# Performance work log

Measured on AMD Instinct MI355X. Metric: run time of the kernel, lower is better.

Reference implementation:

```python
import jax, jax.numpy as jnp
import numpy as np

CUTOFF = 5.0
RBF_DIM = 32
M0, M1, M2 = 128, 64, 32          # node multiplicities for l=0,1,2
DIM_NODE = M0 + 3 * M1 + 5 * M2   # 480
MSG = 64                          # message multiplicity per l
NBLK = 3
MAX_Z = 100


def _sph_harm(d):
    # component-normalized real spherical harmonics up to lmax=2; d: [E,3] unit vectors
    x, y, z = d[:, 0], d[:, 1], d[:, 2]
    s3, s5, s15 = jnp.sqrt(3.0), jnp.sqrt(5.0), jnp.sqrt(15.0)
    return jnp.stack([
        jnp.ones_like(x),
        s3 * x, s3 * y, s3 * z,
        s15 * x * y, s15 * y * z, 0.5 * s5 * (3.0 * z * z - 1.0),
        s15 * x * z, 0.5 * s15 * (x * x - y * y),
    ], axis=-1)  # [E, 9]


def _rbf(d):
    centers = jnp.linspace(0.0, CUTOFF, RBF_DIM)
    width = CUTOFF / (RBF_DIM - 1)
    return jnp.exp(-0.5 * ((d[:, None] - centers) / width) ** 2)  # [E, RBF_DIM]


def _irrep_norm(x):
    # per-node RMS norm of each irrep block (l=0,1,2)
    eps = 1e-6
    parts = []
    for off, mul, dim in ((0, M0, 1), (M0, M1, 3), (M0 + 3 * M1, M2, 5)):
        blk = x[:, off:off + mul * dim].reshape(-1, mul, dim)
        rms = jnp.sqrt(jnp.mean(jnp.sum(blk * blk, axis=-1), axis=-1, keepdims=True) + eps)
        parts.append((blk / rms[..., None]).reshape(-1, mul * dim))
    return jnp.concatenate(parts, axis=-1)


def setup_inputs() -> dict:
    key = jax.random.key(0)
    ks = jax.random.split(key, 20)
    B, N, E = 32, 128, 131072
    BN = B * N

    z = jax.random.randint(ks[0], (B, N), 1, MAX_Z + 1)
    mask = jnp.ones((B, N), jnp.float32)
    edge_src = jax.random.randint(ks[1], (E,), 0, BN)
    edge_dst = jax.random.randint(ks[2], (E,), 0, BN)
    edge_weight = jax.random.uniform(ks[3], (E,), minval=0.1, maxval=CUTOFF)
    ed = jax.random.normal(ks[4], (E, 3), jnp.float32)
    ed = ed / jnp.linalg.norm(ed, axis=-1, keepdims=True)
    edge_vec = ed * edge_weight[:, None]

    def nrm(k, shape, fan_in):
        return jax.random.normal(k, shape, jnp.float32) / np.sqrt(fan_in)

    params = {
        "z_emb": jax.random.normal(ks[5], (MAX_Z + 1, M0), jnp.float32),
        "W_in": nrm(ks[6], (M0, M0), M0),
        "Wp": nrm(ks[7], (NBLK, M0, 3 * MSG), M0),
        "rW1": nrm(ks[8], (NBLK, RBF_DIM, 64), RBF_DIM),
        "rb1": jnp.zeros((NBLK, 64), jnp.float32),
        "rW2": nrm(ks[9], (NBLK, 64, 3 * MSG), 64),
        "rb2": jnp.zeros((NBLK, 3 * MSG), jnp.float32),
        "Wo0": nrm(ks[10], (NBLK, MSG, M0), MSG),
        "Wo1": nrm(ks[11], (NBLK, MSG, M1), MSG),
        "Wo2": nrm(ks[12], (NBLK, MSG, M2), MSG),
        "res_scale": jnp.full((NBLK,), 1.0, jnp.float32),
    }
    return {"z": z, "mask": mask, "edge_src": edge_src, "edge_dst": edge_dst,
            "edge_weight": edge_weight, "edge_vec": edge_vec, **params}


def reference(z, mask, edge_src, edge_dst, edge_weight, edge_vec,
              z_emb, W_in, Wp, rW1, rb1, rW2, rb2, Wo0, Wo1, Wo2, res_scale):
    B, N = z.shape
    BN = B * N
    fmask = mask.reshape(BN)

    # element embedding -> o3.Linear(0e -> irreps_node): only scalar channels are produced
    zf = z_emb[z.reshape(BN)]                                    # [BN, node_attr]
    x0 = zf @ W_in                                               # [BN, M0]
    x = jnp.concatenate([x0, jnp.zeros((BN, DIM_NODE - M0), x0.dtype)], axis=-1)
    x = x * fmask[:, None]

    elen = edge_weight
    edir = edge_vec / jnp.clip(elen, 1e-8)[:, None]
    rbf = _rbf(jnp.minimum(elen, CUTOFF))                        # [E, RBF_DIM]
    sh = _sph_harm(edir)                                         # [E, 9]
    fcut = 0.5 * (jnp.cos(jnp.pi * jnp.minimum(elen / CUTOFF, 1.0)) + 1.0)

    for b in range(NBLK):
        s = x[:, :M0]
        proj = s[edge_src] @ Wp[b]                               # [E, 3*MSG] gather + GEMM
        h = jax.nn.silu(rbf @ rW1[b] + rb1[b])
        r = h @ rW2[b] + rb2[b]                                  # [E, 3*MSG] radial weights
        w = proj * r * fcut[:, None]
        w0, w1, w2 = w[:, :MSG], w[:, MSG:2 * MSG], w[:, 2 * MSG:]
        msg0 = w0 * sh[:, 0:1]                                   # [E, MSG]
        msg1 = w1[:, :, None] * sh[:, None, 1:4]                 # [E, MSG, 3]
        msg2 = w2[:, :, None] * sh[:, None, 4:9]                 # [E, MSG, 5]
        m0 = jax.ops.segment_sum(msg0, edge_dst, num_segments=BN)
        m1 = jax.ops.segment_sum(msg1, edge_dst, num_segments=BN)
        m2 = jax.ops.segment_sum(msg2, edge_dst, num_segments=BN)
        u0 = m0 @ Wo0[b]                                         # [BN, M0]
        u1 = jnp.einsum('ncd,ck->nkd', m1, Wo1[b]).reshape(BN, 3 * M1)
        u2 = jnp.einsum('ncd,ck->nkd', m2, Wo2[b]).reshape(BN, 5 * M2)
        x = x + res_scale[b] * jnp.concatenate([u0, u1, u2], axis=-1)

    x = _irrep_norm(x) * fmask[:, None]
    return x.reshape(B, N, DIM_NODE)
```

## Files before the change

### kernel.cpp

```cpp
#include <hip/hip_runtime.h>
#include <math.h>

#define M0 128
#define M1 64
#define M2 32
#define DIMN 480
#define MSGC 64
#define NBLK 3
#define RBFD 32
#define NT 512
#define TCHUNK 32
#define NNP0 4
#define GNPB 4
#define PSTR 68
#define WROWS 224
#define FCUT 5.0f

typedef unsigned int   u32;
typedef unsigned short u16;

__device__ __forceinline__ u16 f2bf(float f) {
    u32 u = __float_as_uint(f);
    u32 r = (u + 0x7fffu + ((u >> 16) & 1u)) >> 16;
    return (u16)r;
}
__device__ __forceinline__ float bf_lo(u32 v) { return __uint_as_float(v << 16); }
__device__ __forceinline__ float bf_hi(u32 v) { return __uint_as_float(v & 0xffff0000u); }

struct __align__(16) ERec {
    int   src;
    int   ti;
    float fr;
    float fc;
    float sh[8];
};

__global__ void k_zero(int* __restrict__ p, int n) {
    int i = blockIdx.x * blockDim.x + threadIdx.x;
    if (i < n) p[i] = 0;
}

__global__ void k_count(const int* __restrict__ dst, int* __restrict__ counts, int E) {
    int e = blockIdx.x * blockDim.x + threadIdx.x;
    if (e >= E) return;
    atomicAdd(&counts[dst[e]], 1);
}

__global__ __launch_bounds__(1024) void k_scan(const int* __restrict__ counts,
                                               int* __restrict__ offs,
                                               int* __restrict__ cursor, int n) {
    __shared__ int ws[1024];
    int t = threadIdx.x;
    int4 v = ((const int4*)counts)[t];
    int s0 = v.x, s1 = s0 + v.y, s2 = s1 + v.z, s3 = s2 + v.w;
    ws[t] = s3;
    __syncthreads();
    for (int d = 1; d < 1024; d <<= 1) {
        int val = (t >= d) ? ws[t - d] : 0;
        __syncthreads();
        ws[t] += val;
        __syncthreads();
    }
    int excl = (t == 0) ? 0 : ws[t - 1];
    int4 o;
    o.x = excl; o.y = excl + s0; o.z = excl + s1; o.w = excl + s2;
    ((int4*)offs)[t] = o;
    ((int4*)cursor)[t] = o;
    if (t == 1023) offs[n] = excl + s3;
}

__global__ void k_build(const float* __restrict__ ew, const float* __restrict__ ev,
                        const int* __restrict__ src, const int* __restrict__ dst,
                        int* __restrict__ cursor, ERec* __restrict__ rec, int E) {
    int e = blockIdx.x * blockDim.x + threadIdx.x;
    if (e >= E) return;
    float len = ew[e];
    float inv = 1.0f / fmaxf(len, 1e-8f);
    float x = ev[e * 3 + 0] * inv;
    float y = ev[e * 3 + 1] * inv;
    float z = ev[e * 3 + 2] * inv;
    const float s3 = 1.7320508075688772f, s5 = 2.23606797749979f, s15 = 3.872983346207417f;
    ERec r;
    r.src = src[e];
    float u = fminf(len, FCUT) * ((float)(NT - 1) / FCUT);
    int ti = (int)u;
    ti = min(ti, NT - 2);
    r.ti = ti;
    r.fr = u - (float)ti;
    float t = fminf(len / FCUT, 1.0f);
    float fc = 0.5f * (cosf(3.14159265358979323846f * t) + 1.0f);
    r.fc = fc;
    r.sh[0] = s3 * x * fc;
    r.sh[1] = s3 * y * fc;
    r.sh[2] = s3 * z * fc;
    r.sh[3] = s15 * x * y * fc;
    r.sh[4] = s15 * y * z * fc;
    r.sh[5] = 0.5f * s5 * (3.0f * z * z - 1.0f) * fc;
    r.sh[6] = s15 * x * z * fc;
    r.sh[7] = 0.5f * s15 * (x * x - y * y) * fc;
    int p = atomicAdd(&cursor[dst[e]], 1);
    rec[p] = r;
}

#define RTB (NBLK * (NT / TCHUNK))
__global__ __launch_bounds__(256) void k_rtab(const float* __restrict__ rW1,
                                              const float* __restrict__ rb1,
                                              const float* __restrict__ rW2,
                                              const float* __restrict__ rb2,
                                              u32* __restrict__ rPI,
                                              const float* __restrict__ Wo0,
                                              const float* __restrict__ Wo1,
                                              const float* __restrict__ Wo2,
                                              float* __restrict__ WoT) {
    int blk = blockIdx.x;
    int tid = threadIdx.x;
    if (blk >= RTB) {
        int idx = (blk - RTB) * 256 + tid;
        const int wtot = NBLK * WROWS * 64;
        if (idx >= wtot) return;
        int b = idx / (WROWS * 64);
        int rem = idx - b * (WROWS * 64);
        int row = rem >> 6, c = rem & 63;
        float v;
        if (row < 128)      v = Wo0[(size_t)b * MSGC * M0 + c * M0 + row];
        else if (row < 192) v = Wo1[(size_t)b * MSGC * M1 + c * M1 + (row - 128)];
        else                v = Wo2[(size_t)b * MSGC * M2 + c * M2 + (row - 192)];
        WoT[idx] = v;
        return;
    }
    int b = blk / (NT / TCHUNK);
    int t0 = (blk % (NT / TCHUNK)) * TCHUNK;
    __shared__ float rbf_s[TCHUNK + 1][RBFD];
    __shared__ float hh_s[64][TCHUNK + 1];

    const float wdt = FCUT / (float)(RBFD - 1);
    for (int idx = tid; idx < (TCHUNK + 1) * RBFD; idx += 256) {
        int tt = idx >> 5, k = idx & 31;
        int te = min(t0 + tt, NT - 1);
        float len = (float)te * (FCUT / (float)(NT - 1));
        float d0 = (len - (float)k * wdt) / wdt;
        rbf_s[tt][k] = expf(-0.5f * d0 * d0);
    }
    __syncthreads();
    const float* W1 = rW1 + b * RBFD * 64;
    for (int idx = tid; idx < (TCHUNK + 1) * 64; idx += 256) {
        int tt = idx / 64, jj = idx & 63;
        float a = rb1[b * 64 + jj];
        #pragma unroll 8
        for (int k = 0; k < RBFD; ++k) a += rbf_s[tt][k] * W1[k * 64 + jj];
        hh_s[jj][tt] = a / (1.0f + expf(-a));
    }
    __syncthreads();
    if (tid < 192) {
        int c = tid;
        const float* W2 = rW2 + b * 64 * 192;
        float w2r[64];
        #pragma unroll
        for (int k = 0; k < 64; ++k) w2r[k] = W2[k * 192 + c];
        float b2 = rb2[b * 192 + c];
        int lane = c & 63, q = c >> 6;
        u32* out = rPI + ((size_t)b * NT * 64) * 4;
        float prev = 0.0f;
        for (int tt = 0; tt <= TCHUNK; ++tt) {
            float acc = b2;
            #pragma unroll
            for (int k = 0; k < 64; ++k) acc += hh_s[k][tt] * w2r[k];
            if (tt > 0) {
                int t = t0 + tt - 1;
                out[((size_t)t * 64 + lane) * 4 + q] =
                    (u32)f2bf(prev) | ((u32)f2bf(acc) << 16);
            }
            prev = acc;
        }
    }
}

__global__ __launch_bounds__(192) void k_proj0(const int* __restrict__ z,
                                               const float* __restrict__ mask,
                                               const float* __restrict__ zemb,
                                               const float* __restrict__ Win,
                                               const float* __restrict__ Wp,
                                               float* __restrict__ x,
                                               u16* __restrict__ PI) {
    int n0 = blockIdx.x * NNP0;
    int j = threadIdx.x;
    __shared__ float zf[NNP0][M0];
    __shared__ float xs[NNP0][M0];
    for (int idx = j; idx < NNP0 * M0; idx += 192) {
        int n = idx >> 7, c = idx & 127;
        zf[n][c] = zemb[z[n0 + n] * M0 + c];
    }
    __syncthreads();
    for (int idx = j; idx < NNP0 * M0; idx += 192) {
        int n = idx >> 7, c = idx & 127;
        float acc = 0.0f;
        for (int k = 0; k < M0; ++k) acc += zf[n][k] * Win[k * M0 + c];
        acc *= mask[n0 + n];
        xs[n][c] = acc;
        x[(size_t)(n0 + n) * DIMN + c] = acc;
    }
    for (int idx = j; idx < NNP0 * (DIMN - M0); idx += 192) {
        int n = idx / (DIMN - M0), c = idx - n * (DIMN - M0);
        x[(size_t)(n0 + n) * DIMN + M0 + c] = 0.0f;
    }
    __syncthreads();
    float acc[NNP0];
    #pragma unroll
    for (int u = 0; u < NNP0; ++u) acc[u] = 0.0f;
    for (int k = 0; k < M0; ++k) {
        float wv = Wp[k * 192 + j];
        #pragma unroll
        for (int u = 0; u < NNP0; ++u) acc[u] += xs[u][k] * wv;
    }
    int lane = j & 63, q = j >> 6;
    #pragma unroll
    for (int u = 0; u < NNP0; ++u)
        PI[((size_t)(n0 + u) * 64 + lane) * 4 + q] = f2bf(acc[u]);
}

__global__ __launch_bounds__(512) void k_gather(const u16* __restrict__ PIin,
                                                u16* __restrict__ PIout,
                                                const u32* __restrict__ rPI,
                                                const ERec* __restrict__ rec,
                                                const int* __restrict__ offs,
                                                const float* __restrict__ WoT,
                                                const float* __restrict__ WpNext,
                                                const float* __restrict__ res_scale, int b,
                                                float* __restrict__ x,
                                                const float* __restrict__ mask,
                                                float* __restrict__ out) {
    int t = threadIdx.x;
    int w = t >> 6;
    int j = t & 63;
    int local = w >> 1;
    int par = w & 1;
    int n0 = blockIdx.x * GNPB;
    int n = n0 + local;
    int e0 = offs[n], e1 = offs[n + 1];

    float m0 = 0.0f;
    float m1a[3] = {0, 0, 0};
    float m2a[5] = {0, 0, 0, 0, 0};

    __shared__ float mbuf[8][9 * PSTR];
    __shared__ float invs[GNPB][3];

    {
        int i0 = e0 + par;
        if (i0 < e1) {
            const int last = e1 - 1;
            int nIter = (e1 - i0 + 1) >> 1;
            float4 A0, A1, A2, B0, B1, B2, C0, C1, C2;
            {
                int ia = __builtin_amdgcn_readfirstlane(i0);
                const float4* p = (const float4*)(rec + ia);
                A0 = p[0]; A1 = p[1]; A2 = p[2];
            }
            {
                int v = i0 + 2; v = v < e1 ? v : last;
                int ib = __builtin_amdgcn_readfirstlane(v);
                const float4* p = (const float4*)(rec + ib);
                B0 = p[0]; B1 = p[1]; B2 = p[2];
            }
            {
                int v = i0 + 4; v = v < e1 ? v : last;
                int ic = __builtin_amdgcn_readfirstlane(v);
                const float4* p = (const float4*)(rec + ic);
                C0 = p[0]; C1 = p[1]; C2 = p[2];
            }
            uint4 rA, rB, rC; uint2 pA, pB, pC;
            {
                int s = __float_as_int(A0.x), ti = __float_as_int(A0.y);
                rA = ((const uint4*)(rPI + ((size_t)ti << 8)))[j];
                pA = ((const uint2*)(PIin + ((size_t)s << 8)))[j];
            }
            {
                int s = __float_as_int(B0.x), ti = __float_as_int(B0.y);
                rB = ((const uint4*)(rPI + ((size_t)ti << 8)))[j];
                pB = ((const uint2*)(PIin + ((size_t)s << 8)))[j];
            }
            #pragma unroll 4
            for (int k = 0; k < nIter; ++k) {
                int i = i0 + (k << 1);
                float4 D0, D1, D2;
                {
                    int v = i + 6; v = v < e1 ? v : last;
                    int id = __builtin_amdgcn_readfirstlane(v);
                    const float4* p = (const float4*)(rec + id);
                    D0 = p[0]; D1 = p[1]; D2 = p[2];
                }
                {
                    int s = __float_as_int(C0.x), ti = __float_as_int(C0.y);
                    rC = ((const uint4*)(rPI + ((size_t)ti << 8)))[j];
                    pC = ((const uint2*)(PIin + ((size_t)s << 8)))[j];
                }
                float fr = A0.z, fc = A0.w;
                float la = bf_lo(rA.x);
                float va = la + fr * (bf_hi(rA.x) - la);
                float p0 = __uint_as_float(pA.x << 16);
                float p1 = __uint_as_float(pA.x & 0xffff0000u);
                float p2 = __uint_as_float(pA.y << 16);
                m0 = fmaf(p0 * va, fc, m0);
                float lb = bf_lo(rA.y);
                float vb = lb + fr * (bf_hi(rA.y) - lb);
                float w1 = p1 * vb;
                m1a[0] += w1 * A1.x;
                m1a[1] += w1 * A1.y;
                m1a[2] += w1 * A1.z;
                float lc = bf_lo(rA.z);
                float vc = lc + fr * (bf_hi(rA.z) - lc);
                float w2 = p2 * vc;
                m2a[0] += w2 * A1.w;
                m2a[1] += w2 * A2.x;
                m2a[2] += w2 * A2.y;
                m2a[3] += w2 * A2.z;
                m2a[4] += w2 * A2.w;
                A0 = B0; A1 = B1; A2 = B2;
                B0 = C0; B1 = C1; B2 = C2;
                C0 = D0; C1 = D1; C2 = D2;
                rA = rB; pA = pB; rB = rC; pB = pC;
            }
        }
    }

    mbuf[w][0 * PSTR + j] = m0;
    #pragma unroll
    for (int d = 0; d < 3; ++d) mbuf[w][(1 + d) * PSTR + j] = m1a[d];
    #pragma unroll
    for (int d = 0; d < 5; ++d) mbuf[w][(4 + d) * PSTR + j] = m2a[d];
    __syncthreads();
    #pragma unroll
    for (int u = 0; u < GNPB; ++u)
        for (int c = t; c < 9 * PSTR; c += 512)
            mbuf[2 * u][c] += mbuf[2 * u + 1][c];
    __syncthreads();

    float rs = res_scale[b];
    int o = t;
    if (o < DIMN) {
        int row, mbase;
        if (o < M0) {
            row = o; mbase = 0;
        } else if (o < M0 + 3 * M1) {
            int q = o - M0, k = q / 3, d = q - 3 * k;
            row = 128 + k; mbase = (1 + d) * PSTR;
        } else {
            int q = o - (M0 + 3 * M1), k = q / 5, d = q - 5 * k;
            row = 192 + k; mbase = (4 + d) * PSTR;
        }
        const float4* Wv = (const float4*)(WoT + (size_t)row * 64);
        float a0 = 0, a1 = 0, a2 = 0, a3 = 0;
        #pragma unroll
        for (int c4 = 0; c4 < 16; ++c4) {
            float4 wv = Wv[c4];
            float4 v0 = *(const float4*)&mbuf[0][mbase + 4 * c4];
            float4 v1 = *(const float4*)&mbuf[2][mbase + 4 * c4];
            float4 v2 = *(const float4*)&mbuf[4][mbase + 4 * c4];
            float4 v3 = *(const float4*)&mbuf[6][mbase + 4 * c4];
            a0 += wv.x * v0.x + wv.y * v0.y + wv.z * v0.z + wv.w * v0.w;
            a1 += wv.x * v1.x + wv.y * v1.y + wv.z * v1.z + wv.w * v1.w;
            a2 += wv.x * v2.x + wv.y * v2.y + wv.z * v2.z + wv.w * v2.w;
            a3 += wv.x * v3.x + wv.y * v3.y + wv.z * v3.z + wv.w * v3.w;
        }
        a0 = x[(size_t)(n0 + 0) * DIMN + o] + rs * a0;
        a1 = x[(size_t)(n0 + 1) * DIMN + o] + rs * a1;
        a2 = x[(size_t)(n0 + 2) * DIMN + o] + rs * a2;
        a3 = x[(size_t)(n0 + 3) * DIMN + o] + rs * a3;
        if (b < NBLK - 1) {
            x[(size_t)(n0 + 0) * DIMN + o] = a0;
            x[(size_t)(n0 + 1) * DIMN + o] = a1;
            x[(size_t)(n0 + 2) * DIMN + o] = a2;
            x[(size_t)(n0 + 3) * DIMN + o] = a3;
            if (o < M0) {
                mbuf[1][o] = a0; mbuf[3][o] = a1; mbuf[5][o] = a2; mbuf[7][o] = a3;
            }
        } else {
            mbuf[1][o] = a0; mbuf[3][o] = a1; mbuf[5][o] = a2; mbuf[7][o] = a3;
        }
    }

    if (b < NBLK - 1) {
        __syncthreads();
        for (int oo = t; oo < GNPB * 192; oo += 512) {
            int u = oo / 192, c = oo - u * 192;
            const float* xf = mbuf[2 * u + 1];
            float acc = 0.0f;
            #pragma unroll 8
            for (int k = 0; k < M0; ++k) acc += xf[k] * WpNext[k * 192 + c];
            PIout[((size_t)(n0 + u) * 64 + (c & 63)) * 4 + (c >> 6)] = f2bf(acc);
        }
        return;
    }

    __syncthreads();
    if (w < GNPB) {
        const float* xf = mbuf[2 * w + 1];
        float s0 = 0, s1 = 0, s2 = 0;
        for (int c = j; c < DIMN; c += 64) {
            float v = xf[c];
            if (c < 128) s0 += v * v;
            else if (c < 320) s1 += v * v;
            else s2 += v * v;
        }
        #pragma unroll
        for (int d = 32; d > 0; d >>= 1) {
            s0 += __shfl_down(s0, d);
            s1 += __shfl_down(s1, d);
            s2 += __shfl_down(s2, d);
        }
        if (j == 0) {
            invs[w][0] = rsqrtf(s0 / (float)M0 + 1e-6f);
            invs[w][1] = rsqrtf(s1 / (float)M1 + 1e-6f);
            invs[w][2] = rsqrtf(s2 / (float)M2 + 1e-6f);
        }
    }
    __syncthreads();
    if (o < DIMN) {
        int cls = (o < 128) ? 0 : (o < 320) ? 1 : 2;
        #pragma unroll
        for (int u = 0; u < GNPB; ++u) {
            float fm = mask[n0 + u];
            out[(size_t)(n0 + u) * DIMN + o] = mbuf[2 * u + 1][o] * invs[u][cls] * fm;
        }
    }
}

extern "C" void kernel_launch(void* const* d_in, const int* in_sizes, int n_in,
                              void* d_out, int out_size, void* d_ws, size_t ws_size,
                              hipStream_t stream) {
    const int*   z    = (const int*)d_in[0];
    const float* mask = (const float*)d_in[1];
    const int*   esrc = (const int*)d_in[2];
    const int*   edst = (const int*)d_in[3];
    const float* ew   = (const float*)d_in[4];
    const float* ev   = (const float*)d_in[5];
    const float* zemb = (const float*)d_in[6];
    const float* Win  = (const float*)d_in[7];
    const float* Wp   = (const float*)d_in[8];
    const float* rW1  = (const float*)d_in[9];
    const float* rb1  = (const float*)d_in[10];
    const float* rW2  = (const float*)d_in[11];
    const float* rb2  = (const float*)d_in[12];
    const float* Wo0  = (const float*)d_in[13];
    const float* Wo1  = (const float*)d_in[14];
    const float* Wo2  = (const float*)d_in[15];
    const float* res  = (const float*)d_in[16];

    const int BN = in_sizes[0];
    const int E  = in_sizes[2];

    char* w = (char*)d_ws;
    float* x    = (float*)w;  w += (size_t)BN * DIMN * 4;
    u16*   PIa  = (u16*)w;    w += (size_t)BN * 256 * 2;
    u16*   PIb  = (u16*)w;    w += (size_t)BN * 256 * 2;
    u32*   rPI  = (u32*)w;    w += (size_t)NBLK * NT * 256 * 4;
    ERec*  rec  = (ERec*)w;   w += (size_t)E * sizeof(ERec);
    float* WoT  = (float*)w;  w += (size_t)NBLK * WROWS * 64 * 4;
    int* counts = (int*)w;   w += (size_t)BN * 4;
    int* offs   = (int*)w;   w += (size_t)(BN + 4) * 4;
    int* cursor = (int*)w;   w += (size_t)BN * 4;

    k_zero<<<(BN + 255) / 256, 256, 0, stream>>>(counts, BN);
    k_count<<<(E + 255) / 256, 256, 0, stream>>>(edst, counts, E);
    k_scan<<<1, 1024, 0, stream>>>(counts, offs, cursor, BN);
    k_build<<<(E + 255) / 256, 256, 0, stream>>>(ew, ev, esrc, edst, cursor, rec, E);
    {
        int wotb = (NBLK * WROWS * 64 + 255) / 256;
        k_rtab<<<RTB + wotb, 256, 0, stream>>>(rW1, rb1, rW2, rb2, rPI,
                                               Wo0, Wo1, Wo2, WoT);
    }
    k_proj0<<<BN / NNP0, 192, 0, stream>>>(z, mask, zemb, Win, Wp, x, PIa);

    u16* pibuf[2] = {PIa, PIb};
    for (int b = 0; b < NBLK; ++b) {
        const float* WpNext = Wp + (size_t)(b + 1 < NBLK ? b + 1 : 0) * M0 * 192;
        k_gather<<<BN / GNPB, 512, 0, stream>>>(pibuf[b & 1], pibuf[(b + 1) & 1],
                                                rPI + (size_t)b * NT * 256,
                                                rec, offs,
                                                WoT + (size_t)b * WROWS * 64,
                                                WpNext, res, b, x, mask, (float*)d_out);
    }
}
```

Measured before the change: 201.7 us.

## Stage edge records in double-buffered LDS chunks and split edges contiguously per wave

Each wave now loads its edge records cooperatively in chunks of 21 into a double-buffered LDS array, instead of making per-edge scalar global loads with a deep register rotation. Edges are split into two contiguous halves per wave pair rather than interleaved by parity. The change also adds a launch-bounds occupancy hint of 6 and halves TCHUNK. It aims to cut scalar load latency and register pressure, at the cost of extra LDS traffic and chunk-boundary pipeline restarts that reissue the first two gathers of each chunk.

```diff
diff --git a/kernel.cpp b/kernel.cpp
--- a/kernel.cpp
+++ b/kernel.cpp
@@ -9,11 +9,12 @@
 #define NBLK 3
 #define RBFD 32
 #define NT 512
-#define TCHUNK 32
+#define TCHUNK 16
 #define NNP0 4
 #define GNPB 4
 #define PSTR 68
 #define WROWS 224
+#define CH 21
 #define FCUT 5.0f
 
 typedef unsigned int   u32;
@@ -218,17 +219,17 @@
         PI[((size_t)(n0 + u) * 64 + lane) * 4 + q] = f2bf(acc[u]);
 }
 
-__global__ __launch_bounds__(512) void k_gather(const u16* __restrict__ PIin,
-                                                u16* __restrict__ PIout,
-                                                const u32* __restrict__ rPI,
-                                                const ERec* __restrict__ rec,
-                                                const int* __restrict__ offs,
-                                                const float* __restrict__ WoT,
-                                                const float* __restrict__ WpNext,
-                                                const float* __restrict__ res_scale, int b,
-                                                float* __restrict__ x,
-                                                const float* __restrict__ mask,
-                                                float* __restrict__ out) {
+__global__ __launch_bounds__(512, 6) void k_gather(const u16* __restrict__ PIin,
+                                                   u16* __restrict__ PIout,
+                                                   const u32* __restrict__ rPI,
+                                                   const ERec* __restrict__ rec,
+                                                   const int* __restrict__ offs,
+                                                   const float* __restrict__ WoT,
+                                                   const float* __restrict__ WpNext,
+                                                   const float* __restrict__ res_scale, int b,
+                                                   float* __restrict__ x,
+                                                   const float* __restrict__ mask,
+                                                   float* __restrict__ out) {
     int t = threadIdx.x;
     int w = t >> 6;
     int j = t & 63;
@@ -242,83 +243,80 @@
     float m1a[3] = {0, 0, 0};
     float m2a[5] = {0, 0, 0, 0, 0};
 
+    __shared__ float4 smeta[8][2][CH * 3];
     __shared__ float mbuf[8][9 * PSTR];
     __shared__ float invs[GNPB][3];
 
     {
-        int i0 = e0 + par;
-        if (i0 < e1) {
-            const int last = e1 - 1;
-            int nIter = (e1 - i0 + 1) >> 1;
-            float4 A0, A1, A2, B0, B1, B2, C0, C1, C2;
+        int half = (e1 - e0 + 1) >> 1;
+        int a    = e0 + par * half;
+        int bnd  = par ? e1 : (e0 + half);
+        int len  = bnd - a;
+        if (len > 0) {
+            const float4* RP = (const float4*)rec;
             {
-                int ia = __builtin_amdgcn_readfirstlane(i0);
-                const float4* p = (const float4*)(rec + ia);
-                A0 = p[0]; A1 = p[1]; A2 = p[2];
+                int c0 = min(CH, len);
+                if (j < c0 * 3) smeta[w][0][j] = RP[(size_t)3 * a + j];
             }
-            {
-                int v = i0 + 2; v = v < e1 ? v : last;
-                int ib = __builtin_amdgcn_readfirstlane(v);
-                const float4* p = (const float4*)(rec + ib);
-                B0 = p[0]; B1 = p[1]; B2 = p[2];
-            }
-            {
-                int v = i0 + 4; v = v < e1 ? v : last;
-                int ic = __builtin_amdgcn_readfirstlane(v);
-                const float4* p = (const float4*)(rec + ic);
-                C0 = p[0]; C1 = p[1]; C2 = p[2];
-            }
-            uint4 rA, rB, rC; uint2 pA, pB, pC;
-            {
-                int s = __float_as_int(A0.x), ti = __float_as_int(A0.y);
-                rA = ((const uint4*)(rPI + ((size_t)ti << 8)))[j];
-                pA = ((const uint2*)(PIin + ((size_t)s << 8)))[j];
-            }
-            {
-                int s = __float_as_int(B0.x), ti = __float_as_int(B0.y);
-                rB = ((const uint4*)(rPI + ((size_t)ti << 8)))[j];
-                pB = ((const uint2*)(PIin + ((size_t)s << 8)))[j];
-            }
-            #pragma unroll 4
-            for (int k = 0; k < nIter; ++k) {
-                int i = i0 + (k << 1);
-                float4 D0, D1, D2;
+            int buf = 0;
+            for (int done = 0; done < len; done += CH, buf ^= 1) {
+                int cnt = min(CH, len - done);
                 {
-                    int v = i + 6; v = v < e1 ? v : last;
-                    int id = __builtin_amdgcn_readfirstlane(v);
-                    const float4* p = (const float4*)(rec + id);
-                    D0 = p[0]; D1 = p[1]; D2 = p[2];
+                    int nd = done + CH;
+                    int ncnt = min(CH, len - nd);
+                    if (j < ncnt * 3) smeta[w][buf ^ 1][j] = RP[(size_t)3 * (a + nd) + j];
+                }
+                const float4* M = smeta[w][buf];
+                int lastE = cnt - 1;
+                float4 Am = M[0];
+                float4 Bm = M[3 * min(1, lastE)];
+                float4 Cm = M[3 * min(2, lastE)];
+                float4 Dm = M[3 * min(3, lastE)];
+                uint4 rA, rB, rC; uint2 pA, pB, pC;
+                {
+                    int s = __float_as_int(Am.x), ti = __float_as_int(Am.y);
+                    rA = ((const uint4*)(rPI + ((size_t)ti << 8)))[j];
+                    pA = ((const uint2*)(PIin + ((size_t)s << 8)))[j];
                 }
                 {
-                    int s = __float_as_int(C0.x), ti = __float_as_int(C0.y);
-                    rC = ((const uint4*)(rPI + ((size_t)ti << 8)))[j];
-                    pC = ((const uint2*)(PIin + ((size_t)s << 8)))[j];
+                    int s = __float_as_int(Bm.x), ti = __float_as_int(Bm.y);
+                    rB = ((const uint4*)(rPI + ((size_t)ti << 8)))[j];
+                    pB = ((const uint2*)(PIin + ((size_t)s << 8)))[j];
                 }
-                float fr = A0.z, fc = A0.w;
-                float la = bf_lo(rA.x);
-                float va = la + fr * (bf_hi(rA.x) - la);
-                float p0 = __uint_as_float(pA.x << 16);
-                float p1 = __uint_as_float(pA.x & 0xffff0000u);
-                float p2 = __uint_as_float(pA.y << 16);
-                m0 = fmaf(p0 * va, fc, m0);
-                float lb = bf_lo(rA.y);
-                float vb = lb + fr * (bf_hi(rA.y) - lb);
-                float w1 = p1 * vb;
-                m1a[0] += w1 * A1.x;
-                m1a[1] += w1 * A1.y;
-                m1a[2] += w1 * A1.z;
-                float lc = bf_lo(rA.z);
-                float vc = lc + fr * (bf_hi(rA.z) - lc);
-                float w2 = p2 * vc;
-                m2a[0] += w2 * A1.w;
-                m2a[1] += w2 * A2.x;
-                m2a[2] += w2 * A2.y;
-                m2a[3] += w2 * A2.z;
-                m2a[4] += w2 * A2.w;
-                A0 = B0; A1 = B1; A2 = B2;
-                B0 = C0; B1 = C1; B2 = C2;
-                C0 = D0; C1 = D1; C2 = D2;
-                rA = rB; pA = pB; rB = rC; pB = pC;
+                #pragma unroll 3
+                for (int i = 0; i < cnt; ++i) {
+                    {
+                        int s = __float_as_int(Cm.x), ti = __float_as_int(Cm.y);
+                        rC = ((const uint4*)(rPI + ((size_t)ti << 8)))[j];
+                        pC = ((const uint2*)(PIin + ((size_t)s << 8)))[j];
+                    }
+                    float4 Em = M[3 * min(i + 4, lastE)];
+                    float4 S1 = M[3 * i + 1];
+                    float4 S2 = M[3 * i + 2];
+                    float fr = Am.z, fc = Am.w;
+                    float la = bf_lo(rA.x);
+                    float va = la + fr * (bf_hi(rA.x) - la);
+                    float p0 = __uint_as_float(pA.x << 16);
+                    float p1 = __uint_as_float(pA.x & 0xffff0000u);
+                    float p2 = __uint_as_float(pA.y << 16);
+                    m0 = fmaf(p0 * va, fc, m0);
+                    float lb = bf_lo(rA.y);
+                    float vb = lb + fr * (bf_hi(rA.y) - lb);
+                    float w1 = p1 * vb;
+                    m1a[0] += w1 * S1.x;
+                    m1a[1] += w1 * S1.y;
+                    m1a[2] += w1 * S1.z;
+                    float lc = bf_lo(rA.z);
+                    float vc = lc + fr * (bf_hi(rA.z) - lc);
+                    float w2 = p2 * vc;
+                    m2a[0] += w2 * S1.w;
+                    m2a[1] += w2 * S2.x;
+                    m2a[2] += w2 * S2.y;
+                    m2a[3] += w2 * S2.z;
+                    m2a[4] += w2 * S2.w;
+                    Am = Bm; Bm = Cm; Cm = Dm; Dm = Em;
+                    rA = rB; pA = pB; rB = rC; pB = pC;
+                }
             }
         }
     }
```

New measurement: 188.2 us. 6.7% less time.
